# Kernel optimization log

Hardware: AMD Instinct MI355X
Metric: run time of the kernel (lower is better)

## Reference

```python
import jax, jax.numpy as jnp
import numpy as np

B = 32768   # batch of states (original forward is per-state; we vmap)
D = 3       # coord_dim

_W_SHAPES = [("w_h0",(3,32)),("w_y0",(3,32)),("w_yu0",(3,3)),("w_u0",(3,32)),
             ("w_h1",(32,32)),("w_z1",(32,32)),("w_zu1",(32,32)),("w_y1",(3,32)),
             ("w_yu1",(32,3)),("w_u1",(32,32)),("w_h2",(32,32)),("w_z2",(32,32)),
             ("w_zu2",(32,32)),("w_y2",(3,32)),("w_yu2",(32,3)),("w_u2",(32,32)),
             ("w_z_out",(32,1)),("w_zu_out",(32,32)),("w_y_out",(3,1)),
             ("w_yu_out",(32,3)),("w_u_out",(32,1))]
_B_SHAPES = [("b_y0",(3,)),("b_h0",(32,)),("b_0",(32,)),("b_h1",(32,)),("b_y1",(3,)),
             ("b_z1",(32,)),("b_1",(32,)),("b_h2",(32,)),("b_z2",(32,)),("b_y2",(3,)),
             ("b_2",(32,)),("b_z_out",(32,)),("b_y_out",(3,)),("b_out",(1,))]

def _make_params(key):
    n = len(_W_SHAPES) + len(_B_SHAPES) + 4
    ks = jax.random.split(key, n)
    p, i = {}, 0
    for name, sh in _W_SHAPES:   # torch .uniform_(-0.1, 0.1)
        p[name] = jax.random.uniform(ks[i], sh, jnp.float32, -0.1, 0.1); i += 1
    for name, sh in _B_SHAPES:   # torch.rand -> U[0,1)
        p[name] = jax.random.uniform(ks[i], sh, jnp.float32, 0.0, 1.0); i += 1
    # fc layers: normal init per _init_weights (stds / sqrt(16)=4), zero bias
    stds = [2.2/4.0, 0.58/4.0, 0.58*2.0/4.0, 4.0]
    shapes = [(32, 3), (32, 32), (32, 32), (1, 32)]
    for j in range(4):
        p[f"fc{j+1}_w"] = stds[j] * jax.random.normal(ks[i], shapes[j], jnp.float32); i += 1
        p[f"fc{j+1}_b"] = jnp.zeros((shapes[j][0],), jnp.float32)
    return p

def setup_inputs():
    key = jax.random.key(0)
    kx, kp = jax.random.split(key)
    inp = {"x": jax.random.normal(kx, (B, 2 * D), jnp.float32)}
    inp.update(_make_params(kp))
    return inp

def _forward(x, p):
    sp, relu = jax.nn.softplus, jax.nn.relu

    def lagr(state):
        q, y = state[:D], state[D:]
        u1 = sp(q @ p["w_h0"] + p["b_h0"])
        z1 = sp((y * (q @ p["w_yu0"] + p["b_y0"])) @ p["w_y0"] + q @ p["w_u0"] + p["b_0"])
        u2 = sp(u1 @ p["w_h1"] + p["b_h1"])
        z2 = sp((z1 * (u1 @ p["w_zu1"] + p["b_z1"])) @ relu(p["w_z1"])
                + (y * (u1 @ p["w_yu1"] + p["b_y1"])) @ p["w_y1"]
                + u1 @ p["w_u1"] + p["b_1"])
        u3 = sp(u2 @ p["w_h2"] + p["b_h2"])
        z3 = sp((z2 * (u2 @ p["w_zu2"] + p["b_z2"])) @ relu(p["w_z2"])
                + (y * (u2 @ p["w_yu2"] + p["b_y2"])) @ p["w_y2"]
                + u2 @ p["w_u2"] + p["b_2"])
        zout = sp((z3 * (u3 @ p["w_zu_out"] + p["b_z_out"])) @ relu(p["w_z_out"])
                  + (y * (u3 @ p["w_yu_out"] + p["b_y_out"])) @ p["w_y_out"]
                  + u3 @ p["w_u_out"] + p["b_out"])
        V = sp(q @ p["fc1_w"].T + p["fc1_b"])
        V = sp(V @ p["fc2_w"].T + p["fc2_b"])
        V = sp(V @ p["fc3_w"].T + p["fc3_b"])
        V = V @ p["fc4_w"].T + p["fc4_b"]
        return (zout - V)[0]  # scalar Lagrangian

    def step(state):
        dq = state[D:]
        H = jax.hessian(lagr)(state)        # (6,6)
        g = jax.grad(lagr)(state)[:D]       # dL/dq, matches jacobian row b[0,:3]
        M = H[D:, D:]                       # d2L/ddq ddq
        C = H[D:, :D]                       # d2L/ddq dq
        ddq = (g - dq @ C.T) @ jnp.linalg.inv(M).T
        dx = jnp.concatenate([dq, ddq])
        return state + 0.001 * dx           # Euler step, as in torch forward

    return jax.vmap(step)(x)

def reference(x, w_h0, w_y0, w_yu0, w_u0, w_h1, w_z1, w_zu1, w_y1, w_yu1, w_u1,
              w_h2, w_z2, w_zu2, w_y2, w_yu2, w_u2, w_z_out, w_zu_out, w_y_out,
              w_yu_out, w_u_out, b_y0, b_h0, b_0, b_h1, b_y1, b_z1, b_1, b_h2,
              b_z2, b_y2, b_2, b_z_out, b_y_out, b_out, fc1_w, fc1_b, fc2_w,
              fc2_b, fc3_w, fc3_b, fc4_w, fc4_b):
    p = dict(locals())
    xv = p.pop("x")
    return _forward(xv, p)
```

## Files before the change

### kernel.cpp

```cpp
#include <hip/hip_runtime.h>

#define NTH 256
#define B_TOTAL 32768

typedef float v2f __attribute__((ext_vector_type(2)));
typedef float v4f __attribute__((ext_vector_type(4)));

struct Ptrs { const float* p[44]; };

enum : int {
  I_X = 0,
  I_WH0 = 1, I_WY0 = 2, I_WYU0 = 3, I_WU0 = 4,
  I_WH1 = 5, I_WZ1 = 6, I_WZU1 = 7, I_WY1 = 8, I_WYU1 = 9, I_WU1 = 10,
  I_WH2 = 11, I_WZ2 = 12, I_WZU2 = 13, I_WY2 = 14, I_WYU2 = 15, I_WU2 = 16,
  I_WZO = 17, I_WZUO = 18, I_WYO = 19, I_WYUO = 20, I_WUO = 21,
  I_BY0 = 22, I_BH0 = 23, I_B0 = 24, I_BH1 = 25, I_BY1 = 26, I_BZ1 = 27, I_B1 = 28,
  I_BH2 = 29, I_BZ2 = 30, I_BY2 = 31, I_B2 = 32, I_BZO = 33, I_BYO = 34, I_BOUT = 35,
  I_FC1 = 36, I_FC1B = 37, I_FC2 = 38, I_FC2B = 39, I_FC3 = 40, I_FC3B = 41,
  I_FC4 = 42, I_FC4B = 43
};

struct V22 { float c[22]; };

__device__ __forceinline__ float spf(float x) {
  return fmaxf(x, 0.0f) + __logf(1.0f + __expf(-fabsf(x)));
}
__device__ __forceinline__ float sigf(float x) {
  return __fdividef(1.0f, 1.0f + __expf(-x));
}

__device__ __forceinline__ V22 spchain22(const V22& A) {
  V22 Z;
  float s = sigf(A.c[0]);
  float d = s * (1.0f - s);
  Z.c[0] = spf(A.c[0]);
#pragma unroll
  for (int a = 0; a < 3; ++a) Z.c[1 + a] = s * A.c[1 + a];
#pragma unroll
  for (int b = 0; b < 3; ++b) Z.c[4 + b] = s * A.c[4 + b];
  const int pa[6] = {0, 0, 0, 1, 1, 2}, pb[6] = {0, 1, 2, 1, 2, 2};
#pragma unroll
  for (int t = 0; t < 6; ++t)
    Z.c[7 + t] = s * A.c[7 + t] + d * A.c[1 + pa[t]] * A.c[1 + pb[t]];
#pragma unroll
  for (int a = 0; a < 3; ++a)
#pragma unroll
    for (int b = 0; b < 3; ++b)
      Z.c[13 + a * 3 + b] = s * A.c[13 + a * 3 + b] + d * A.c[1 + a] * A.c[4 + b];
  return Z;
}

__device__ __forceinline__ void stageProd(float* row, const V22& Z, float S0, float S1,
                                          float S2, float S3) {
  float z0 = Z.c[0];
  v4f w0 = {z0 * S0, S0 * Z.c[1], S0 * Z.c[2], S0 * Z.c[3]};
  v4f w1 = {z0 * S1 + S0 * Z.c[4], z0 * S2 + S0 * Z.c[5], z0 * S3 + S0 * Z.c[6], S0 * Z.c[7]};
  v4f w2 = {S0 * Z.c[8], S0 * Z.c[9], S0 * Z.c[10], S0 * Z.c[11]};
  v4f w3 = {S0 * Z.c[12], S0 * Z.c[13] + Z.c[1] * S1, S0 * Z.c[14] + Z.c[1] * S2,
            S0 * Z.c[15] + Z.c[1] * S3};
  v4f w4 = {S0 * Z.c[16] + Z.c[2] * S1, S0 * Z.c[17] + Z.c[2] * S2, S0 * Z.c[18] + Z.c[2] * S3,
            S0 * Z.c[19] + Z.c[3] * S1};
  v4f w5 = {S0 * Z.c[20] + Z.c[3] * S2, S0 * Z.c[21] + Z.c[3] * S3, 0.0f, 0.0f};
  *(v4f*)(row + 0) = w0;  *(v4f*)(row + 4) = w1;  *(v4f*)(row + 8) = w2;
  *(v4f*)(row + 12) = w3; *(v4f*)(row + 16) = w4; *(v4f*)(row + 20) = w5;
}

__device__ __forceinline__ V22 prodZS(const V22& Z, float S0, float S1, float S2, float S3) {
  V22 P;
  const float Sq[3] = {S1, S2, S3};
  P.c[0] = Z.c[0] * S0;
#pragma unroll
  for (int a = 0; a < 3; ++a) P.c[1 + a] = S0 * Z.c[1 + a];
#pragma unroll
  for (int b = 0; b < 3; ++b) P.c[4 + b] = Z.c[0] * Sq[b] + S0 * Z.c[4 + b];
#pragma unroll
  for (int t = 0; t < 6; ++t) P.c[7 + t] = S0 * Z.c[7 + t];
#pragma unroll
  for (int a = 0; a < 3; ++a)
#pragma unroll
    for (int b = 0; b < 3; ++b)
      P.c[13 + a * 3 + b] = S0 * Z.c[13 + a * 3 + b] + Z.c[1 + a] * Sq[b];
  return P;
}

__device__ __forceinline__ void mvA(const float* __restrict__ W, int j, const float* ps,
                                    v2f& m0, v2f& m1, v2f& m2, v2f& m3, v2f& m4, v2f& m5) {
#pragma unroll 2
  for (int i = 0; i < 32; ++i) {
    float w = fmaxf(W[i * 32 + j], 0.0f);
    const float* r = ps + i * 24;
    v4f r0 = *(const v4f*)(r + 0);
    v4f r1 = *(const v4f*)(r + 4);
    v4f r2 = *(const v4f*)(r + 8);
    m0 += r0.xy * w; m1 += r0.zw * w;
    m2 += r1.xy * w; m3 += r1.zw * w;
    m4 += r2.xy * w; m5 += r2.zw * w;
  }
}
__device__ __forceinline__ void mvB(const float* __restrict__ W, int j, const float* ps,
                                    v2f& m6, v2f& m7, v2f& m8, v2f& m9, v2f& m10) {
#pragma unroll 2
  for (int i = 0; i < 32; ++i) {
    float w = fmaxf(W[i * 32 + j], 0.0f);
    const float* r = ps + i * 24;
    v4f r3 = *(const v4f*)(r + 12);
    v4f r4 = *(const v4f*)(r + 16);
    v2f r5 = *(const v2f*)(r + 20);
    m6 += r3.xy * w; m7 += r3.zw * w;
    m8 += r4.xy * w; m9 += r4.zw * w;
    m10 += r5 * w;
  }
}

__device__ __forceinline__ void stageU_hs(const float* __restrict__ Wh,
                                          const float* __restrict__ Wzu, int j,
                                          const float* us, v2f& h0, v2f& h1, v2f& s0, v2f& s1) {
#pragma unroll 2
  for (int i = 0; i < 32; ++i) {
    v4f u = *(const v4f*)(us + i * 4);
    float wh = Wh[i * 32 + j], wz = Wzu[i * 32 + j];
    h0 += u.xy * wh; h1 += u.zw * wh;
    s0 += u.xy * wz; s1 += u.zw * wz;
  }
}
__device__ __forceinline__ void stageU_wt(const float* __restrict__ Wu,
                                          const float* __restrict__ Wyu, int j,
                                          const float* us, v2f& w0, v2f& w1,
                                          v2f& ta0, v2f& ta1, v2f& tb0, v2f& tb1,
                                          v2f& tc0, v2f& tc1) {
#pragma unroll 2
  for (int i = 0; i < 32; ++i) {
    v4f u = *(const v4f*)(us + i * 4);
    float wu = Wu[i * 32 + j];
    w0 += u.xy * wu; w1 += u.zw * wu;
    float wy0 = Wyu[i * 3 + 0], wy1 = Wyu[i * 3 + 1], wy2 = Wyu[i * 3 + 2];
    ta0 += u.xy * wy0; ta1 += u.zw * wy0;
    tb0 += u.xy * wy1; tb1 += u.zw * wy1;
    tc0 += u.xy * wy2; tc1 += u.zw * wy2;
  }
}

__device__ __forceinline__ void buildA(const float* __restrict__ Wy, int j, float y0, float y1,
                                       float y2, const float wv[4], const float ta[4],
                                       const float tb[4], const float tc[4], V22& A) {
  float wy0 = Wy[j], wy1 = Wy[32 + j], wy2 = Wy[64 + j];
  A.c[0] = wv[0] + y0 * ta[0] * wy0 + y1 * tb[0] * wy1 + y2 * tc[0] * wy2;
  A.c[1] = ta[0] * wy0; A.c[2] = tb[0] * wy1; A.c[3] = tc[0] * wy2;
#pragma unroll
  for (int b = 0; b < 3; ++b)
    A.c[4 + b] = wv[1 + b] + y0 * ta[1 + b] * wy0 + y1 * tb[1 + b] * wy1 + y2 * tc[1 + b] * wy2;
#pragma unroll
  for (int t6 = 0; t6 < 6; ++t6) A.c[7 + t6] = 0.0f;
#pragma unroll
  for (int b = 0; b < 3; ++b) {
    A.c[13 + 0 * 3 + b] = ta[1 + b] * wy0;
    A.c[13 + 1 * 3 + b] = tb[1 + b] * wy1;
    A.c[13 + 2 * 3 + b] = tc[1 + b] * wy2;
  }
}

__global__ __launch_bounds__(NTH, 4) void lnn_step_kernel(Ptrs P, float* __restrict__ out) {
  __shared__ float pstage[4][2][32][24];
  __shared__ float ustage[4][2][32][4];

  const int tid = threadIdx.x;
  const int j = tid & 31;
  const int half = (tid >> 5) & 1;
  const int wv = tid >> 6;
  const int sample = blockIdx.x * 8 + (tid >> 5);

  float* prow = &pstage[wv][half][0][0];
  float* urow = &ustage[wv][half][0][0];

  const float* X = P.p[I_X] + sample * 6;
  const float q0 = X[0], q1 = X[1], q2 = X[2];
  const float y0 = X[3], y1 = X[4], y2 = X[5];

  float Vg0, Vg1, Vg2;
  {
    const float* fc1 = P.p[I_FC1];
    float f0 = fc1[j * 3], f1 = fc1[j * 3 + 1], f2 = fc1[j * 3 + 2];
    float hp = P.p[I_FC1B][j] + q0 * f0 + q1 * f1 + q2 * f2;
    float ss = sigf(hp);
    v4f V1 = {spf(hp), ss * f0, ss * f1, ss * f2};
    *(v4f*)(urow + j * 4) = V1;
    const float* fc2 = P.p[I_FC2] + j * 32;
    v2f a0 = {P.p[I_FC2B][j], 0.0f}, a1 = {0.0f, 0.0f};
#pragma unroll 2
    for (int r = 0; r < 8; ++r) {
      v4f w4 = *(const v4f*)(fc2 + r * 4);
      v4f u0 = *(const v4f*)(urow + (r * 4 + 0) * 4);
      v4f u1 = *(const v4f*)(urow + (r * 4 + 1) * 4);
      v4f u2 = *(const v4f*)(urow + (r * 4 + 2) * 4);
      v4f u3 = *(const v4f*)(urow + (r * 4 + 3) * 4);
      a0 += u0.xy * w4.x; a1 += u0.zw * w4.x;
      a0 += u1.xy * w4.y; a1 += u1.zw * w4.y;
      a0 += u2.xy * w4.z; a1 += u2.zw * w4.z;
      a0 += u3.xy * w4.w; a1 += u3.zw * w4.w;
    }
    float ss2 = sigf(a0.x);
    v4f V2 = {spf(a0.x), ss2 * a0.y, ss2 * a1.x, ss2 * a1.y};
    *(v4f*)(urow + j * 4) = V2;
    const float* fc3 = P.p[I_FC3] + j * 32;
    v2f b0 = {P.p[I_FC3B][j], 0.0f}, b1 = {0.0f, 0.0f};
#pragma unroll 2
    for (int r = 0; r < 8; ++r) {
      v4f w4 = *(const v4f*)(fc3 + r * 4);
      v4f u0 = *(const v4f*)(urow + (r * 4 + 0) * 4);
      v4f u1 = *(const v4f*)(urow + (r * 4 + 1) * 4);
      v4f u2 = *(const v4f*)(urow + (r * 4 + 2) * 4);
      v4f u3 = *(const v4f*)(urow + (r * 4 + 3) * 4);
      b0 += u0.xy * w4.x; b1 += u0.zw * w4.x;
      b0 += u1.xy * w4.y; b1 += u1.zw * w4.y;
      b0 += u2.xy * w4.z; b1 += u2.zw * w4.z;
      b0 += u3.xy * w4.w; b1 += u3.zw * w4.w;
    }
    float ss3 = sigf(b0.x);
    float f4 = P.p[I_FC4][j];
    Vg0 = ss3 * b0.y * f4; Vg1 = ss3 * b1.x * f4; Vg2 = ss3 * b1.y * f4;
  }

  const float* yu0 = P.p[I_WYU0];
  float t0v[3];
#pragma unroll
  for (int k = 0; k < 3; ++k)
    t0v[k] = q0 * yu0[k] + q1 * yu0[3 + k] + q2 * yu0[6 + k] + P.p[I_BY0][k];

  float u1c[4];
  {
    const float* wh0 = P.p[I_WH0];
    float w0 = wh0[j], w1 = wh0[32 + j], w2 = wh0[64 + j];
    float h = P.p[I_BH0][j] + q0 * w0 + q1 * w1 + q2 * w2;
    float ss = sigf(h);
    u1c[0] = spf(h); u1c[1] = ss * w0; u1c[2] = ss * w1; u1c[3] = ss * w2;
  }

  V22 z;
  {
    const float* Wy = P.p[I_WY0];
    const float* Wu = P.p[I_WU0];
    float wy0 = Wy[j], wy1 = Wy[32 + j], wy2 = Wy[64 + j];
    float wu0 = Wu[j], wu1 = Wu[32 + j], wu2 = Wu[64 + j];
    V22 A;
    A.c[0] = P.p[I_B0][j] + (y0 * t0v[0]) * wy0 + (y1 * t0v[1]) * wy1 + (y2 * t0v[2]) * wy2 +
             q0 * wu0 + q1 * wu1 + q2 * wu2;
    A.c[1] = t0v[0] * wy0; A.c[2] = t0v[1] * wy1; A.c[3] = t0v[2] * wy2;
#pragma unroll
    for (int b = 0; b < 3; ++b) {
      float acc = (b == 0 ? wu0 : (b == 1 ? wu1 : wu2));
      acc += y0 * yu0[b * 3 + 0] * wy0 + y1 * yu0[b * 3 + 1] * wy1 + y2 * yu0[b * 3 + 2] * wy2;
      A.c[4 + b] = acc;
    }
#pragma unroll
    for (int t = 0; t < 6; ++t) A.c[7 + t] = 0.0f;
#pragma unroll
    for (int b = 0; b < 3; ++b) {
      A.c[13 + 0 * 3 + b] = yu0[b * 3 + 0] * wy0;
      A.c[13 + 1 * 3 + b] = yu0[b * 3 + 1] * wy1;
      A.c[13 + 2 * 3 + b] = yu0[b * 3 + 2] * wy2;
    }
    z = spchain22(A);
  }

  float unext[4];
#pragma unroll 1
  for (int lvl = 0; lvl < 2; ++lvl) {
    const float* Wh  = P.p[lvl == 0 ? I_WH1 : I_WH2];
    const float* Wzu = P.p[lvl == 0 ? I_WZU1 : I_WZU2];
    const float* Wu  = P.p[lvl == 0 ? I_WU1 : I_WU2];
    const float* Wyu = P.p[lvl == 0 ? I_WYU1 : I_WYU2];
    const float* Wy  = P.p[lvl == 0 ? I_WY1 : I_WY2];
    const float* Wz  = P.p[lvl == 0 ? I_WZ1 : I_WZ2];
    const float* Bh  = P.p[lvl == 0 ? I_BH1 : I_BH2];
    const float* Bz  = P.p[lvl == 0 ? I_BZ1 : I_BZ2];
    const float* Bl  = P.p[lvl == 0 ? I_B1 : I_B2];
    const float* By  = P.p[lvl == 0 ? I_BY1 : I_BY2];

    const float* uc = (lvl == 0) ? u1c : unext;
    v4f uu = {uc[0], uc[1], uc[2], uc[3]};
    *(v4f*)(urow + j * 4) = uu;

    v2f h0 = {Bh[j], 0.0f}, h1 = {0.0f, 0.0f};
    v2f s0 = {Bz[j], 0.0f}, s1 = {0.0f, 0.0f};
    stageU_hs(Wh, Wzu, j, urow, h0, h1, s0, s1);
    {
      float ss = sigf(h0.x);
      unext[0] = spf(h0.x); unext[1] = ss * h0.y; unext[2] = ss * h1.x; unext[3] = ss * h1.y;
    }
    stageProd(prow + j * 24, z, s0.x, s0.y, s1.x, s1.y);

    v2f w0 = {Bl[j], 0.0f}, w1 = {0.0f, 0.0f};
    v2f ta0 = {By[0], 0.0f}, ta1 = {0.0f, 0.0f};
    v2f tb0 = {By[1], 0.0f}, tb1 = {0.0f, 0.0f};
    v2f tc0 = {By[2], 0.0f}, tc1 = {0.0f, 0.0f};
    stageU_wt(Wu, Wyu, j, urow, w0, w1, ta0, ta1, tb0, tb1, tc0, tc1);

    float wvv[4] = {w0.x, w0.y, w1.x, w1.y};
    float tav[4] = {ta0.x, ta0.y, ta1.x, ta1.y};
    float tbv[4] = {tb0.x, tb0.y, tb1.x, tb1.y};
    float tcv[4] = {tc0.x, tc0.y, tc1.x, tc1.y};
    V22 A2;
    buildA(Wy, j, y0, y1, y2, wvv, tav, tbv, tcv, A2);

    v2f m0 = {A2.c[0], A2.c[1]},  m1 = {A2.c[2], A2.c[3]},  m2 = {A2.c[4], A2.c[5]};
    v2f m3 = {A2.c[6], A2.c[7]},  m4 = {A2.c[8], A2.c[9]},  m5 = {A2.c[10], A2.c[11]};
    v2f m6 = {A2.c[12], A2.c[13]}, m7 = {A2.c[14], A2.c[15]}, m8 = {A2.c[16], A2.c[17]};
    v2f m9 = {A2.c[18], A2.c[19]}, m10 = {A2.c[20], A2.c[21]};
    mvA(Wz, j, prow, m0, m1, m2, m3, m4, m5);
    mvB(Wz, j, prow, m6, m7, m8, m9, m10);
    A2.c[0] = m0.x;  A2.c[1] = m0.y;  A2.c[2] = m1.x;  A2.c[3] = m1.y;
    A2.c[4] = m2.x;  A2.c[5] = m2.y;  A2.c[6] = m3.x;  A2.c[7] = m3.y;
    A2.c[8] = m4.x;  A2.c[9] = m4.y;  A2.c[10] = m5.x; A2.c[11] = m5.y;
    A2.c[12] = m6.x; A2.c[13] = m6.y; A2.c[14] = m7.x; A2.c[15] = m7.y;
    A2.c[16] = m8.x; A2.c[17] = m8.y; A2.c[18] = m9.x; A2.c[19] = m9.y;
    A2.c[20] = m10.x; A2.c[21] = m10.y;
    z = spchain22(A2);
  }

  {
    v4f uu = {unext[0], unext[1], unext[2], unext[3]};
    *(v4f*)(urow + j * 4) = uu;
  }
  v2f s30 = {P.p[I_BZO][j], 0.0f}, s31 = {0.0f, 0.0f};
  {
    const float* Wzuo = P.p[I_WZUO];
#pragma unroll 2
    for (int i = 0; i < 32; ++i) {
      v4f u = *(const v4f*)(urow + i * 4);
      float wz = Wzuo[i * 32 + j];
      s30 += u.xy * wz; s31 += u.zw * wz;
    }
  }
  v2f wo0 = {0.0f, 0.0f}, wo1 = {0.0f, 0.0f};
  v2f t3a0 = {P.p[I_BYO][0], 0.0f}, t3a1 = {0.0f, 0.0f};
  v2f t3b0 = {P.p[I_BYO][1], 0.0f}, t3b1 = {0.0f, 0.0f};
  v2f t3c0 = {P.p[I_BYO][2], 0.0f}, t3c1 = {0.0f, 0.0f};
  {
    const float* Wuo = P.p[I_WUO];
    const float* Wyuo = P.p[I_WYUO];
#pragma unroll 2
    for (int i = 0; i < 32; ++i) {
      v4f u = *(const v4f*)(urow + i * 4);
      float wu = Wuo[i];
      wo0 += u.xy * wu; wo1 += u.zw * wu;
      float wy0 = Wyuo[i * 3], wy1 = Wyuo[i * 3 + 1], wy2 = Wyuo[i * 3 + 2];
      t3a0 += u.xy * wy0; t3a1 += u.zw * wy0;
      t3b0 += u.xy * wy1; t3b1 += u.zw * wy1;
      t3c0 += u.xy * wy2; t3c1 += u.zw * wy2;
    }
  }
  const float woc[4] = {wo0.x, wo0.y, wo1.x, wo1.y};
  const float t3av[4] = {t3a0.x, t3a0.y, t3a1.x, t3a1.y};
  const float t3bv[4] = {t3b0.x, t3b0.y, t3b1.x, t3b1.y};
  const float t3cv[4] = {t3c0.x, t3c0.y, t3c1.x, t3c1.y};

  float red[25];
  {
    V22 p3 = prodZS(z, s30.x, s30.y, s31.x, s31.y);
    float wz = fmaxf(P.p[I_WZO][j], 0.0f);
#pragma unroll
    for (int k = 0; k < 22; ++k) red[k] = p3.c[k] * wz;
    red[22] = Vg0; red[23] = Vg1; red[24] = Vg2;
  }
#pragma unroll
  for (int m = 16; m >= 1; m >>= 1) {
#pragma unroll
    for (int k = 0; k < 25; ++k) red[k] += __shfl_xor(red[k], m, 32);
  }

  if (j == 0) {
    const float* Wyo = P.p[I_WYO];
    const float wyo0 = Wyo[0], wyo1 = Wyo[1], wyo2 = Wyo[2];
    float Av = red[0] + woc[0] + P.p[I_BOUT][0] + y0 * t3av[0] * wyo0 +
               y1 * t3bv[0] * wyo1 + y2 * t3cv[0] * wyo2;
    float Agy[3];
    Agy[0] = red[1] + t3av[0] * wyo0;
    Agy[1] = red[2] + t3bv[0] * wyo1;
    Agy[2] = red[3] + t3cv[0] * wyo2;
    float Agq[3];
#pragma unroll
    for (int b = 0; b < 3; ++b)
      Agq[b] = red[4 + b] + woc[1 + b] + y0 * t3av[1 + b] * wyo0 +
               y1 * t3bv[1 + b] * wyo1 + y2 * t3cv[1 + b] * wyo2;
    float s = sigf(Av), d = s * (1.0f - s);

    double Mm[3][3], Cm[3][3];
    const int pa[6] = {0, 0, 0, 1, 1, 2}, pb[6] = {0, 1, 2, 1, 2, 2};
#pragma unroll
    for (int t = 0; t < 6; ++t) {
      double m = (double)s * (double)red[7 + t] +
                 (double)d * (double)Agy[pa[t]] * (double)Agy[pb[t]];
      Mm[pa[t]][pb[t]] = m; Mm[pb[t]][pa[t]] = m;
    }
#pragma unroll
    for (int b = 0; b < 3; ++b) {
      float ah0 = red[13 + 0 * 3 + b] + t3av[1 + b] * wyo0;
      float ah1 = red[13 + 1 * 3 + b] + t3bv[1 + b] * wyo1;
      float ah2 = red[13 + 2 * 3 + b] + t3cv[1 + b] * wyo2;
      Cm[0][b] = (double)s * (double)ah0 + (double)d * (double)Agy[0] * (double)Agq[b];
      Cm[1][b] = (double)s * (double)ah1 + (double)d * (double)Agy[1] * (double)Agq[b];
      Cm[2][b] = (double)s * (double)ah2 + (double)d * (double)Agy[2] * (double)Agq[b];
    }
    const double yd0 = (double)y0, yd1 = (double)y1, yd2 = (double)y2;
    double rr[3];
#pragma unroll
    for (int i2 = 0; i2 < 3; ++i2) {
      double g = (double)s * (double)Agq[i2] - (double)red[22 + i2];
      rr[i2] = g - (yd0 * Cm[i2][0] + yd1 * Cm[i2][1] + yd2 * Cm[i2][2]);
    }
    double a = Mm[0][0], b_ = Mm[0][1], c_ = Mm[0][2], dd = Mm[1][1], e = Mm[1][2], f = Mm[2][2];
    double A00 = dd * f - e * e, A01 = c_ * e - b_ * f, A02 = b_ * e - c_ * dd;
    double A11 = a * f - c_ * c_, A12 = b_ * c_ - a * e, A22 = a * dd - b_ * b_;
    double det = a * A00 + b_ * A01 + c_ * A02;
    double idet = 1.0 / det;
    double d0 = (A00 * rr[0] + A01 * rr[1] + A02 * rr[2]) * idet;
    double d1 = (A01 * rr[0] + A11 * rr[1] + A12 * rr[2]) * idet;
    double d2 = (A02 * rr[0] + A12 * rr[1] + A22 * rr[2]) * idet;

    float* O = out + (size_t)sample * 6;
    O[0] = q0 + 0.001f * y0;
    O[1] = q1 + 0.001f * y1;
    O[2] = q2 + 0.001f * y2;
    O[3] = y0 + 0.001f * (float)d0;
    O[4] = y1 + 0.001f * (float)d1;
    O[5] = y2 + 0.001f * (float)d2;
  }
}

extern "C" void kernel_launch(void* const* d_in, const int* in_sizes, int n_in,
                              void* d_out, int out_size, void* d_ws, size_t ws_size,
                              hipStream_t stream) {
  (void)in_sizes; (void)n_in; (void)d_ws; (void)ws_size; (void)out_size;
  Ptrs P;
  for (int i = 0; i < 44; ++i) P.p[i] = (const float*)d_in[i];
  float* out = (float*)d_out;
  dim3 grid(B_TOTAL / 8), block(NTH);
  hipLaunchKernelGGL(lnn_step_kernel, grid, block, 0, stream, P, out);
}
```

Baseline: 161.5 us.

## Contract mixed Hessian block with velocity early, shrinking propagated jet from 22 to 16

Instead of carrying the full 3x3 mixed second-derivative block (d2/dy dq) through every layer, the kernel carries only its contraction with the velocity y, since only C·y is needed in the final solve. This cuts the forward-mode jet from 22 to 16 components, which reduces shared-memory staging, matrix-vector FMAs, and shuffle reductions. The launch-bounds occupancy hint is doubled to 8 to take advantage of the smaller register and LDS footprint. Summation order changes slightly, and the tighter register budget could cause spills.

Measured after the change: 197.7 us. 22.4% more time.

```diff
diff --git a/kernel.cpp b/kernel.cpp
--- a/kernel.cpp
+++ b/kernel.cpp
@@ -20,7 +20,7 @@
   I_FC4 = 42, I_FC4B = 43
 };
 
-struct V22 { float c[22]; };
+struct V16 { float c[16]; };
 
 __device__ __forceinline__ float spf(float x) {
   return fmaxf(x, 0.0f) + __logf(1.0f + __expf(-fabsf(x)));
@@ -29,8 +29,8 @@
   return __fdividef(1.0f, 1.0f + __expf(-x));
 }
 
-__device__ __forceinline__ V22 spchain22(const V22& A) {
-  V22 Z;
+__device__ __forceinline__ V16 spchain16(const V16& A, float y0, float y1, float y2) {
+  V16 Z;
   float s = sigf(A.c[0]);
   float d = s * (1.0f - s);
   Z.c[0] = spf(A.c[0]);
@@ -38,36 +38,36 @@
   for (int a = 0; a < 3; ++a) Z.c[1 + a] = s * A.c[1 + a];
 #pragma unroll
   for (int b = 0; b < 3; ++b) Z.c[4 + b] = s * A.c[4 + b];
-  const int pa[6] = {0, 0, 0, 1, 1, 2}, pb[6] = {0, 1, 2, 1, 2, 2};
-#pragma unroll
-  for (int t = 0; t < 6; ++t)
-    Z.c[7 + t] = s * A.c[7 + t] + d * A.c[1 + pa[t]] * A.c[1 + pb[t]];
-#pragma unroll
-  for (int a = 0; a < 3; ++a)
-#pragma unroll
-    for (int b = 0; b < 3; ++b)
-      Z.c[13 + a * 3 + b] = s * A.c[13 + a * 3 + b] + d * A.c[1 + a] * A.c[4 + b];
+  Z.c[7]  = s * A.c[7]  + d * A.c[1] * A.c[1];
+  Z.c[8]  = s * A.c[8]  + d * A.c[1] * A.c[2];
+  Z.c[9]  = s * A.c[9]  + d * A.c[1] * A.c[3];
+  Z.c[10] = s * A.c[10] + d * A.c[2] * A.c[2];
+  Z.c[11] = s * A.c[11] + d * A.c[2] * A.c[3];
+  Z.c[12] = s * A.c[12] + d * A.c[3] * A.c[3];
+  float ydq = y0 * A.c[4] + y1 * A.c[5] + y2 * A.c[6];
+#pragma unroll
+  for (int a = 0; a < 3; ++a) Z.c[13 + a] = s * A.c[13 + a] + d * A.c[1 + a] * ydq;
   return Z;
 }
 
-__device__ __forceinline__ void stageProd(float* row, const V22& Z, float S0, float S1,
-                                          float S2, float S3) {
+__device__ __forceinline__ void stageProd(float* row, const V16& Z, float S0, float S1,
+                                          float S2, float S3, float y0, float y1, float y2) {
   float z0 = Z.c[0];
+  float ysd = y0 * S1 + y1 * S2 + y2 * S3;
   v4f w0 = {z0 * S0, S0 * Z.c[1], S0 * Z.c[2], S0 * Z.c[3]};
   v4f w1 = {z0 * S1 + S0 * Z.c[4], z0 * S2 + S0 * Z.c[5], z0 * S3 + S0 * Z.c[6], S0 * Z.c[7]};
   v4f w2 = {S0 * Z.c[8], S0 * Z.c[9], S0 * Z.c[10], S0 * Z.c[11]};
-  v4f w3 = {S0 * Z.c[12], S0 * Z.c[13] + Z.c[1] * S1, S0 * Z.c[14] + Z.c[1] * S2,
-            S0 * Z.c[15] + Z.c[1] * S3};
-  v4f w4 = {S0 * Z.c[16] + Z.c[2] * S1, S0 * Z.c[17] + Z.c[2] * S2, S0 * Z.c[18] + Z.c[2] * S3,
-            S0 * Z.c[19] + Z.c[3] * S1};
-  v4f w5 = {S0 * Z.c[20] + Z.c[3] * S2, S0 * Z.c[21] + Z.c[3] * S3, 0.0f, 0.0f};
-  *(v4f*)(row + 0) = w0;  *(v4f*)(row + 4) = w1;  *(v4f*)(row + 8) = w2;
-  *(v4f*)(row + 12) = w3; *(v4f*)(row + 16) = w4; *(v4f*)(row + 20) = w5;
-}
-
-__device__ __forceinline__ V22 prodZS(const V22& Z, float S0, float S1, float S2, float S3) {
-  V22 P;
+  v4f w3 = {S0 * Z.c[12], S0 * Z.c[13] + Z.c[1] * ysd, S0 * Z.c[14] + Z.c[2] * ysd,
+            S0 * Z.c[15] + Z.c[3] * ysd};
+  *(v4f*)(row + 0) = w0;  *(v4f*)(row + 4) = w1;
+  *(v4f*)(row + 8) = w2;  *(v4f*)(row + 12) = w3;
+}
+
+__device__ __forceinline__ V16 prodZS16(const V16& Z, float S0, float S1, float S2, float S3,
+                                        float y0, float y1, float y2) {
+  V16 P;
   const float Sq[3] = {S1, S2, S3};
+  float ysd = y0 * S1 + y1 * S2 + y2 * S3;
   P.c[0] = Z.c[0] * S0;
 #pragma unroll
   for (int a = 0; a < 3; ++a) P.c[1 + a] = S0 * Z.c[1 + a];
@@ -76,39 +76,25 @@
 #pragma unroll
   for (int t = 0; t < 6; ++t) P.c[7 + t] = S0 * Z.c[7 + t];
 #pragma unroll
-  for (int a = 0; a < 3; ++a)
-#pragma unroll
-    for (int b = 0; b < 3; ++b)
-      P.c[13 + a * 3 + b] = S0 * Z.c[13 + a * 3 + b] + Z.c[1 + a] * Sq[b];
+  for (int a = 0; a < 3; ++a) P.c[13 + a] = S0 * Z.c[13 + a] + Z.c[1 + a] * ysd;
   return P;
 }
 
-__device__ __forceinline__ void mvA(const float* __restrict__ W, int j, const float* ps,
-                                    v2f& m0, v2f& m1, v2f& m2, v2f& m3, v2f& m4, v2f& m5) {
+__device__ __forceinline__ void mv16(const float* __restrict__ W, int j, const float* ps,
+                                     v2f& m0, v2f& m1, v2f& m2, v2f& m3,
+                                     v2f& m4, v2f& m5, v2f& m6, v2f& m7) {
 #pragma unroll 2
   for (int i = 0; i < 32; ++i) {
     float w = fmaxf(W[i * 32 + j], 0.0f);
-    const float* r = ps + i * 24;
+    const float* r = ps + i * 16;
     v4f r0 = *(const v4f*)(r + 0);
     v4f r1 = *(const v4f*)(r + 4);
     v4f r2 = *(const v4f*)(r + 8);
+    v4f r3 = *(const v4f*)(r + 12);
     m0 += r0.xy * w; m1 += r0.zw * w;
     m2 += r1.xy * w; m3 += r1.zw * w;
     m4 += r2.xy * w; m5 += r2.zw * w;
-  }
-}
-__device__ __forceinline__ void mvB(const float* __restrict__ W, int j, const float* ps,
-                                    v2f& m6, v2f& m7, v2f& m8, v2f& m9, v2f& m10) {
-#pragma unroll 2
-  for (int i = 0; i < 32; ++i) {
-    float w = fmaxf(W[i * 32 + j], 0.0f);
-    const float* r = ps + i * 24;
-    v4f r3 = *(const v4f*)(r + 12);
-    v4f r4 = *(const v4f*)(r + 16);
-    v2f r5 = *(const v2f*)(r + 20);
     m6 += r3.xy * w; m7 += r3.zw * w;
-    m8 += r4.xy * w; m9 += r4.zw * w;
-    m10 += r5 * w;
   }
 }
 
@@ -140,9 +126,9 @@
   }
 }
 
-__device__ __forceinline__ void buildA(const float* __restrict__ Wy, int j, float y0, float y1,
-                                       float y2, const float wv[4], const float ta[4],
-                                       const float tb[4], const float tc[4], V22& A) {
+__device__ __forceinline__ void buildA16(const float* __restrict__ Wy, int j, float y0, float y1,
+                                         float y2, const float wv[4], const float ta[4],
+                                         const float tb[4], const float tc[4], V16& A) {
   float wy0 = Wy[j], wy1 = Wy[32 + j], wy2 = Wy[64 + j];
   A.c[0] = wv[0] + y0 * ta[0] * wy0 + y1 * tb[0] * wy1 + y2 * tc[0] * wy2;
   A.c[1] = ta[0] * wy0; A.c[2] = tb[0] * wy1; A.c[3] = tc[0] * wy2;
@@ -151,16 +137,14 @@
     A.c[4 + b] = wv[1 + b] + y0 * ta[1 + b] * wy0 + y1 * tb[1 + b] * wy1 + y2 * tc[1 + b] * wy2;
 #pragma unroll
   for (int t6 = 0; t6 < 6; ++t6) A.c[7 + t6] = 0.0f;
-#pragma unroll
-  for (int b = 0; b < 3; ++b) {
-    A.c[13 + 0 * 3 + b] = ta[1 + b] * wy0;
-    A.c[13 + 1 * 3 + b] = tb[1 + b] * wy1;
-    A.c[13 + 2 * 3 + b] = tc[1 + b] * wy2;
-  }
-}
-
-__global__ __launch_bounds__(NTH, 4) void lnn_step_kernel(Ptrs P, float* __restrict__ out) {
-  __shared__ float pstage[4][2][32][24];
+  float yta = y0 * ta[1] + y1 * ta[2] + y2 * ta[3];
+  float ytb = y0 * tb[1] + y1 * tb[2] + y2 * tb[3];
+  float ytc = y0 * tc[1] + y1 * tc[2] + y2 * tc[3];
+  A.c[13] = yta * wy0; A.c[14] = ytb * wy1; A.c[15] = ytc * wy2;
+}
+
+__global__ __launch_bounds__(NTH, 8) void lnn_step_kernel(Ptrs P, float* __restrict__ out) {
+  __shared__ float pstage[4][2][32][16];
   __shared__ float ustage[4][2][32][4];
 
   const int tid = threadIdx.x;
@@ -235,13 +219,13 @@
     u1c[0] = spf(h); u1c[1] = ss * w0; u1c[2] = ss * w1; u1c[3] = ss * w2;
   }
 
-  V22 z;
+  V16 z;
   {
     const float* Wy = P.p[I_WY0];
     const float* Wu = P.p[I_WU0];
     float wy0 = Wy[j], wy1 = Wy[32 + j], wy2 = Wy[64 + j];
     float wu0 = Wu[j], wu1 = Wu[32 + j], wu2 = Wu[64 + j];
-    V22 A;
+    V16 A;
     A.c[0] = P.p[I_B0][j] + (y0 * t0v[0]) * wy0 + (y1 * t0v[1]) * wy1 + (y2 * t0v[2]) * wy2 +
              q0 * wu0 + q1 * wu1 + q2 * wu2;
     A.c[1] = t0v[0] * wy0; A.c[2] = t0v[1] * wy1; A.c[3] = t0v[2] * wy2;
@@ -253,13 +237,11 @@
     }
 #pragma unroll
     for (int t = 0; t < 6; ++t) A.c[7 + t] = 0.0f;
-#pragma unroll
-    for (int b = 0; b < 3; ++b) {
-      A.c[13 + 0 * 3 + b] = yu0[b * 3 + 0] * wy0;
-      A.c[13 + 1 * 3 + b] = yu0[b * 3 + 1] * wy1;
-      A.c[13 + 2 * 3 + b] = yu0[b * 3 + 2] * wy2;
-    }
-    z = spchain22(A);
+    float yty0 = y0 * yu0[0] + y1 * yu0[3] + y2 * yu0[6];
+    float yty1 = y0 * yu0[1] + y1 * yu0[4] + y2 * yu0[7];
+    float yty2 = y0 * yu0[2] + y1 * yu0[5] + y2 * yu0[8];
+    A.c[13] = yty0 * wy0; A.c[14] = yty1 * wy1; A.c[15] = yty2 * wy2;
+    z = spchain16(A, y0, y1, y2);
   }
 
   float unext[4];
@@ -287,7 +269,7 @@
       float ss = sigf(h0.x);
       unext[0] = spf(h0.x); unext[1] = ss * h0.y; unext[2] = ss * h1.x; unext[3] = ss * h1.y;
     }
-    stageProd(prow + j * 24, z, s0.x, s0.y, s1.x, s1.y);
+    stageProd(prow + j * 16, z, s0.x, s0.y, s1.x, s1.y, y0, y1, y2);
 
     v2f w0 = {Bl[j], 0.0f}, w1 = {0.0f, 0.0f};
     v2f ta0 = {By[0], 0.0f}, ta1 = {0.0f, 0.0f};
@@ -299,22 +281,19 @@
     float tav[4] = {ta0.x, ta0.y, ta1.x, ta1.y};
     float tbv[4] = {tb0.x, tb0.y, tb1.x, tb1.y};
     float tcv[4] = {tc0.x, tc0.y, tc1.x, tc1.y};
-    V22 A2;
-    buildA(Wy, j, y0, y1, y2, wvv, tav, tbv, tcv, A2);
-
-    v2f m0 = {A2.c[0], A2.c[1]},  m1 = {A2.c[2], A2.c[3]},  m2 = {A2.c[4], A2.c[5]};
-    v2f m3 = {A2.c[6], A2.c[7]},  m4 = {A2.c[8], A2.c[9]},  m5 = {A2.c[10], A2.c[11]};
-    v2f m6 = {A2.c[12], A2.c[13]}, m7 = {A2.c[14], A2.c[15]}, m8 = {A2.c[16], A2.c[17]};
-    v2f m9 = {A2.c[18], A2.c[19]}, m10 = {A2.c[20], A2.c[21]};
-    mvA(Wz, j, prow, m0, m1, m2, m3, m4, m5);
-    mvB(Wz, j, prow, m6, m7, m8, m9, m10);
+    V16 A2;
+    buildA16(Wy, j, y0, y1, y2, wvv, tav, tbv, tcv, A2);
+
+    v2f m0 = {A2.c[0], A2.c[1]},   m1 = {A2.c[2], A2.c[3]};
+    v2f m2 = {A2.c[4], A2.c[5]},   m3 = {A2.c[6], A2.c[7]};
+    v2f m4 = {A2.c[8], A2.c[9]},   m5 = {A2.c[10], A2.c[11]};
+    v2f m6 = {A2.c[12], A2.c[13]}, m7 = {A2.c[14], A2.c[15]};
+    mv16(Wz, j, prow, m0, m1, m2, m3, m4, m5, m6, m7);
     A2.c[0] = m0.x;  A2.c[1] = m0.y;  A2.c[2] = m1.x;  A2.c[3] = m1.y;
     A2.c[4] = m2.x;  A2.c[5] = m2.y;  A2.c[6] = m3.x;  A2.c[7] = m3.y;
     A2.c[8] = m4.x;  A2.c[9] = m4.y;  A2.c[10] = m5.x; A2.c[11] = m5.y;
     A2.c[12] = m6.x; A2.c[13] = m6.y; A2.c[14] = m7.x; A2.c[15] = m7.y;
-    A2.c[16] = m8.x; A2.c[17] = m8.y; A2.c[18] = m9.x; A2.c[19] = m9.y;
-    A2.c[20] = m10.x; A2.c[21] = m10.y;
-    z = spchain22(A2);
+    z = spchain16(A2, y0, y1, y2);
   }
 
   {
@@ -354,18 +333,18 @@
   const float t3bv[4] = {t3b0.x, t3b0.y, t3b1.x, t3b1.y};
   const float t3cv[4] = {t3c0.x, t3c0.y, t3c1.x, t3c1.y};
 
-  float red[25];
-  {
-    V22 p3 = prodZS(z, s30.x, s30.y, s31.x, s31.y);
+  float red[19];
+  {
+    V16 p3 = prodZS16(z, s30.x, s30.y, s31.x, s31.y, y0, y1, y2);
     float wz = fmaxf(P.p[I_WZO][j], 0.0f);
 #pragma unroll
-    for (int k = 0; k < 22; ++k) red[k] = p3.c[k] * wz;
-    red[22] = Vg0; red[23] = Vg1; red[24] = Vg2;
+    for (int k = 0; k < 16; ++k) red[k] = p3.c[k] * wz;
+    red[16] = Vg0; red[17] = Vg1; red[18] = Vg2;
   }
 #pragma unroll
   for (int m = 16; m >= 1; m >>= 1) {
 #pragma unroll
-    for (int k = 0; k < 25; ++k) red[k] += __shfl_xor(red[k], m, 32);
+    for (int k = 0; k < 19; ++k) red[k] += __shfl_xor(red[k], m, 32);
   }
 
   if (j == 0) {
@@ -382,9 +361,13 @@
     for (int b = 0; b < 3; ++b)
       Agq[b] = red[4 + b] + woc[1 + b] + y0 * t3av[1 + b] * wyo0 +
                y1 * t3bv[1 + b] * wyo1 + y2 * t3cv[1 + b] * wyo2;
+    float ycq[3];
+    ycq[0] = red[13] + (y0 * t3av[1] + y1 * t3av[2] + y2 * t3av[3]) * wyo0;
+    ycq[1] = red[14] + (y0 * t3bv[1] + y1 * t3bv[2] + y2 * t3bv[3]) * wyo1;
+    ycq[2] = red[15] + (y0 * t3cv[1] + y1 * t3cv[2] + y2 * t3cv[3]) * wyo2;
     float s = sigf(Av), d = s * (1.0f - s);
 
-    double Mm[3][3], Cm[3][3];
+    double Mm[3][3];
     const int pa[6] = {0, 0, 0, 1, 1, 2}, pb[6] = {0, 1, 2, 1, 2, 2};
 #pragma unroll
     for (int t = 0; t < 6; ++t) {
@@ -392,21 +375,14 @@
                  (double)d * (double)Agy[pa[t]] * (double)Agy[pb[t]];
       Mm[pa[t]][pb[t]] = m; Mm[pb[t]][pa[t]] = m;
     }
-#pragma unroll
-    for (int b = 0; b < 3; ++b) {
-      float ah0 = red[13 + 0 * 3 + b] + t3av[1 + b] * wyo0;
-      float ah1 = red[13 + 1 * 3 + b] + t3bv[1 + b] * wyo1;
-      float ah2 = red[13 + 2 * 3 + b] + t3cv[1 + b] * wyo2;
-      Cm[0][b] = (double)s * (double)ah0 + (double)d * (double)Agy[0] * (double)Agq[b];
-      Cm[1][b] = (double)s * (double)ah1 + (double)d * (double)Agy[1] * (double)Agq[b];
-      Cm[2][b] = (double)s * (double)ah2 + (double)d * (double)Agy[2] * (double)Agq[b];
-    }
-    const double yd0 = (double)y0, yd1 = (double)y1, yd2 = (double)y2;
+    double yAgq = (double)y0 * (double)Agq[0] + (double)y1 * (double)Agq[1] +
+                  (double)y2 * (double)Agq[2];
     double rr[3];
 #pragma unroll
-    for (int i2 = 0; i2 < 3; ++i2) {
-      double g = (double)s * (double)Agq[i2] - (double)red[22 + i2];
-      rr[i2] = g - (yd0 * Cm[i2][0] + yd1 * Cm[i2][1] + yd2 * Cm[i2][2]);
+    for (int a = 0; a < 3; ++a) {
+      double g = (double)s * (double)Agq[a] - (double)red[16 + a];
+      double Cy = (double)s * (double)ycq[a] + (double)d * (double)Agy[a] * yAgq;
+      rr[a] = g - Cy;
     }
     double a = Mm[0][0], b_ = Mm[0][1], c_ = Mm[0][2], dd = Mm[1][1], e = Mm[1][2], f = Mm[2][2];
     double A00 = dd * f - e * e, A01 = c_ * e - b_ * f, A02 = b_ * e - c_ * dd;
```
